# Optimization experiments

Hardware: AMD Instinct MI355X
Metric: run time of the kernel (lower is better)

## Reference

```python
import jax, jax.numpy as jnp
import numpy as np

S, DIM, H = 2048, 1024, 16
D = DIM // H  # head_dim = 64


def rope_rotate_half(x):
    x1, x2 = jnp.split(x, 2, axis=-1)
    return jnp.concatenate([-x2, x1], axis=-1)


def setup_inputs() -> dict:
    key = jax.random.key(0)
    ks = jax.random.split(key, 8)
    x = jax.random.normal(ks[0], (S, DIM), dtype=jnp.float32)
    # RoPE tables for full sequence (HW == S, prefix == 0)
    pos = jnp.arange(S, dtype=jnp.float32)[:, None]
    inv_freq = 1.0 / (10000.0 ** (jnp.arange(0, D, 2, dtype=jnp.float32) / D))
    ang = pos * inv_freq[None, :]                      # [S, D/2]
    ang = jnp.concatenate([ang, ang], axis=-1)         # [S, D]
    sin, cos = jnp.sin(ang), jnp.cos(ang)
    # equinox Linear: weight [out, in], y = W @ x + b
    W_qkv = jax.random.normal(ks[1], (3 * DIM, DIM), dtype=jnp.float32) * (DIM ** -0.5)
    b_qkv = jnp.zeros((3 * DIM,), dtype=jnp.float32)
    W_proj = jax.random.normal(ks[2], (DIM, DIM), dtype=jnp.float32) * (DIM ** -0.5)
    b_proj = jnp.zeros((DIM,), dtype=jnp.float32)
    return {"x": x, "sin": sin, "cos": cos, "W_qkv": W_qkv, "b_qkv": b_qkv,
            "W_proj": W_proj, "b_proj": b_proj}


def reference(x, sin, cos, W_qkv, b_qkv, W_proj, b_proj):
    # fused QKV projection: [S, 3*DIM]
    qkv = x @ W_qkv.T + b_qkv
    # 's (n h d) -> n h s d'
    qkv = qkv.reshape(S, 3, H, D).transpose(1, 2, 0, 3)
    q, k, v = qkv[0], qkv[1], qkv[2]                   # each [H, S, D]
    # qk_norm = False -> Identity. RoPE over all S tokens (prefix = 0).
    sin_b, cos_b = sin[None, :, :], cos[None, :, :]    # [1, S, D]
    q = q * cos_b + rope_rotate_half(q) * sin_b
    k = k * cos_b + rope_rotate_half(k) * sin_b
    attn = jnp.einsum('hqd,hkd->hqk', q, k) / jnp.sqrt(jnp.float32(D))
    attn = jax.nn.softmax(attn, axis=-1)               # [H, S, S]
    out = jnp.einsum('hqk,hkd->hqd', attn, v)          # [H, S, D]
    out = out.transpose(1, 0, 2).reshape(S, DIM)       # 'h s d -> s (h d)'
    return out @ W_proj.T + b_proj
```

## Files before the change

### kernel.cpp

```cpp
#include <hip/hip_runtime.h>

#define S_LEN 2048
#define DIM 1024
#define NH 16
#define HD 64
#define KSPLIT 4

typedef __attribute__((ext_vector_type(8))) __bf16 bf16x8;
typedef __attribute__((ext_vector_type(4))) _Float16 f16x4;
typedef __attribute__((ext_vector_type(4))) float f32x4;
typedef __attribute__((ext_vector_type(8))) unsigned short us8;
typedef __attribute__((ext_vector_type(4))) unsigned short us4;

__device__ __forceinline__ unsigned short f2bf(float f) {
    union { float f; unsigned u; } v; v.f = f;
    unsigned r = v.u + 0x7FFFu + ((v.u >> 16) & 1u);
    return (unsigned short)(r >> 16);
}
__device__ __forceinline__ f32x4 mfma16(bf16x8 a, bf16x8 b, f32x4 c) {
    return __builtin_amdgcn_mfma_f32_16x16x32_bf16(a, b, c, 0, 0, 0);
}
__device__ __forceinline__ f32x4 mfma16h(f16x4 a, f16x4 b, f32x4 c) {
    return __builtin_amdgcn_mfma_f32_16x16x16f16(a, b, c, 0, 0, 0);
}
__device__ __forceinline__ void gload_lds16(void* lds, const void* g) {
    __builtin_amdgcn_global_load_lds(
        (__attribute__((address_space(1))) void*)const_cast<void*>(g),
        (__attribute__((address_space(3))) void*)lds, 16, 0, 0);
}

__global__ __launch_bounds__(256) void convert3_kernel(
    const float* __restrict__ a, unsigned short* __restrict__ oa,
    const float* __restrict__ b, unsigned short* __restrict__ ob,
    const float* __restrict__ c, unsigned short* __restrict__ oc)
{
    const int bid = blockIdx.x;
    const float* in;
    unsigned short* out;
    int i;
    if (bid < 1024)      { in = a; out = oa; i = (bid * 256 + threadIdx.x) * 8; }
    else if (bid < 2560) { in = b; out = ob; i = ((bid - 1024) * 256 + threadIdx.x) * 8; }
    else                 { in = c; out = oc; i = ((bid - 2560) * 256 + threadIdx.x) * 8; }
    const float4 p = *(const float4*)(in + i);
    const float4 q = *(const float4*)(in + i + 4);
    us8 o;
    o[0] = f2bf(p.x); o[1] = f2bf(p.y); o[2] = f2bf(p.z); o[3] = f2bf(p.w);
    o[4] = f2bf(q.x); o[5] = f2bf(q.y); o[6] = f2bf(q.z); o[7] = f2bf(q.w);
    *(us8*)(out + i) = o;
}

__global__ __launch_bounds__(256) void gemm_n128_kernel(
    const unsigned short* __restrict__ A, const unsigned short* __restrict__ B,
    const float* __restrict__ bias, float* __restrict__ C,
    int M, int N, int K)
{
    __shared__ __align__(16) unsigned short As[128 * 32];
    __shared__ __align__(16) unsigned short Bs[128 * 32];

    const int tid  = threadIdx.x;
    const int w    = tid >> 6;
    const int lane = tid & 63;
    const int quad = lane >> 4;
    const int l15  = lane & 15;
    const int bm = blockIdx.y * 128, bn = blockIdx.x * 128;
    const int wm = (w >> 1) * 64,    wn = (w & 1) * 64;
    const int srow = lane >> 2;
    const int skc  = (lane & 3) * 8;

    f32x4 acc[4][4];
    const f32x4 zero4 = {0.f, 0.f, 0.f, 0.f};
    #pragma unroll
    for (int i = 0; i < 4; ++i)
        #pragma unroll
        for (int j = 0; j < 4; ++j) acc[i][j] = zero4;

    for (int k0 = 0; k0 < K; k0 += 32) {
        __syncthreads();
        #pragma unroll
        for (int t = 0; t < 2; ++t) {
            const int row = w * 32 + t * 16 + srow;
            const int ldsoff = (w * 32 + t * 16) * 32;
            gload_lds16(&As[ldsoff], A + (size_t)(bm + row) * K + k0 + skc);
            gload_lds16(&Bs[ldsoff], B + (size_t)(bn + row) * K + k0 + skc);
        }
        __syncthreads();

        bf16x8 a[4], b[4];
        #pragma unroll
        for (int i = 0; i < 4; ++i) {
            a[i] = *(const bf16x8*)&As[(wm + 16 * i + l15) * 32 + quad * 8];
            b[i] = *(const bf16x8*)&Bs[(wn + 16 * i + l15) * 32 + quad * 8];
        }
        #pragma unroll
        for (int i = 0; i < 4; ++i)
            #pragma unroll
            for (int j = 0; j < 4; ++j)
                acc[i][j] = mfma16(a[i], b[j], acc[i][j]);
    }

    #pragma unroll
    for (int j = 0; j < 4; ++j) {
        const int col = bn + wn + 16 * j + l15;
        const float bv = bias[col];
        #pragma unroll
        for (int i = 0; i < 4; ++i)
            #pragma unroll
            for (int r = 0; r < 4; ++r) {
                const int row = bm + wm + 16 * i + quad * 4 + r;
                C[(size_t)row * N + col] = acc[i][j][r] + bv;
            }
    }
}

__global__ __launch_bounds__(256) void gemm_n64_kernel(
    const unsigned short* __restrict__ A, const unsigned short* __restrict__ B,
    const float* __restrict__ bias, float* __restrict__ C,
    int M, int N, int K)
{
    __shared__ __align__(16) unsigned short As[128 * 32];
    __shared__ __align__(16) unsigned short Bs[64 * 32];

    const int tid  = threadIdx.x;
    const int w    = tid >> 6;
    const int lane = tid & 63;
    const int quad = lane >> 4;
    const int l15  = lane & 15;
    const int bm = blockIdx.y * 128, bn = blockIdx.x * 64;
    const int wm = w * 32;
    const int srow = lane >> 2;
    const int skc  = (lane & 3) * 8;

    f32x4 acc[2][4];
    const f32x4 zero4 = {0.f, 0.f, 0.f, 0.f};
    #pragma unroll
    for (int i = 0; i < 2; ++i)
        #pragma unroll
        for (int j = 0; j < 4; ++j) acc[i][j] = zero4;

    for (int k0 = 0; k0 < K; k0 += 32) {
        __syncthreads();
        #pragma unroll
        for (int t = 0; t < 2; ++t) {
            const int row = w * 32 + t * 16 + srow;
            gload_lds16(&As[(w * 32 + t * 16) * 32],
                        A + (size_t)(bm + row) * K + k0 + skc);
        }
        gload_lds16(&Bs[(w * 16) * 32],
                    B + (size_t)(bn + w * 16 + srow) * K + k0 + skc);
        __syncthreads();

        bf16x8 a[2], b[4];
        #pragma unroll
        for (int i = 0; i < 2; ++i)
            a[i] = *(const bf16x8*)&As[(wm + 16 * i + l15) * 32 + quad * 8];
        #pragma unroll
        for (int j = 0; j < 4; ++j)
            b[j] = *(const bf16x8*)&Bs[(16 * j + l15) * 32 + quad * 8];
        #pragma unroll
        for (int i = 0; i < 2; ++i)
            #pragma unroll
            for (int j = 0; j < 4; ++j)
                acc[i][j] = mfma16(a[i], b[j], acc[i][j]);
    }

    #pragma unroll
    for (int j = 0; j < 4; ++j) {
        const int col = bn + 16 * j + l15;
        const float bv = bias[col];
        #pragma unroll
        for (int i = 0; i < 2; ++i)
            #pragma unroll
            for (int r = 0; r < 4; ++r) {
                const int row = bm + wm + 16 * i + quad * 4 + r;
                C[(size_t)row * N + col] = acc[i][j][r] + bv;
            }
    }
}

__global__ __launch_bounds__(256) void rope_vtrans_kernel(
    const float* __restrict__ qkv, const float* __restrict__ sin_t,
    const float* __restrict__ cos_t, unsigned short* __restrict__ Qbf,
    unsigned short* __restrict__ Kbf, _Float16* __restrict__ Vt)
{
    const int bid = blockIdx.x;
    if (bid < 8192) {
        const int idx = bid * 256 + threadIdx.x;
        const int s  = idx >> 10;
        const int r  = idx & 1023;
        const int qk = r >> 9;
        const int h  = (r >> 5) & 15;
        const int d  = r & 31;
        const size_t base = (size_t)s * (3 * DIM) + qk * DIM + h * HD + d;
        const float a = qkv[base];
        const float b = qkv[base + 32];
        const float sv = sin_t[s * HD + d];
        const float cv = cos_t[s * HD + d];
        float ra = a * cv - b * sv;
        float rb = b * cv + a * sv;
        unsigned short* dst = qk ? Kbf : Qbf;
        if (!qk) { ra *= 0.125f; rb *= 0.125f; }
        const size_t o = (size_t)h * S_LEN * HD + (size_t)s * HD + d;
        dst[o]      = f2bf(ra);
        dst[o + 32] = f2bf(rb);
    } else {
        const int vb = bid - 8192;
        const int h  = vb >> 7;
        const int sb = (vb & 127) * 16;
        const int d  = threadIdx.x & 63;
        const int sc = threadIdx.x >> 6;
        const int s0 = sb + sc * 4;
        f16x4 o;
        #pragma unroll
        for (int i = 0; i < 4; ++i)
            o[i] = (_Float16)(qkv[(size_t)(s0 + i) * (3 * DIM) + 2 * DIM + h * HD + d]);
        *(f16x4*)&Vt[(size_t)h * HD * S_LEN + (size_t)d * S_LEN + s0] = o;
    }
}

__global__ __launch_bounds__(256, 4) void attn_mfma_kernel(
    const unsigned short* __restrict__ Qbf, const unsigned short* __restrict__ Kbf,
    const _Float16* __restrict__ Vt, float* __restrict__ Opart,
    float* __restrict__ Lpart)
{
    __shared__ __align__(16) unsigned short Ks[64 * 64];
    __shared__ __align__(16) unsigned short Vts[64 * 64];

    const int h   = blockIdx.y;
    const int qb  = blockIdx.x * 128;
    const int ks  = blockIdx.z;
    const int kb0 = ks * (S_LEN / KSPLIT);
    const int tid  = threadIdx.x;
    const int w    = tid >> 6;
    const int lane = tid & 63;
    const int quad = lane >> 4;
    const int l15  = lane & 15;
    const int t7   = l15 & 7;
    const size_t hoff = (size_t)h * S_LEN * HD;

    bf16x8 aq[2][2];
    #pragma unroll
    for (int g = 0; g < 2; ++g)
        #pragma unroll
        for (int c = 0; c < 2; ++c)
            aq[g][c] = *(const bf16x8*)
                &Qbf[hoff + (size_t)(qb + w * 32 + g * 16 + l15) * HD + 32 * c + quad * 8];

    const f32x4 zero4 = {0.f, 0.f, 0.f, 0.f};
    f32x4 o[2][4];
    #pragma unroll
    for (int g = 0; g < 2; ++g)
        #pragma unroll
        for (int dt = 0; dt < 4; ++dt) o[g][dt] = zero4;
    float lsum[2] = {0.f, 0.f};

    const int r0 = tid >> 3;
    const int c0 = tid & 7;

    for (int kb = 0; kb < S_LEN / KSPLIT; kb += 64) {
        __syncthreads();
        #pragma unroll
        for (int i = 0; i < 2; ++i) {
            const int row = r0 + 32 * i;
            const int sw  = ((c0 ^ (row & 7)) << 3);
            *(us8*)&Ks[row * 64 + sw] =
                *(const us8*)&Kbf[hoff + (size_t)(kb0 + kb + row) * HD + c0 * 8];
            *(us8*)&Vts[row * 64 + sw] =
                *(const us8*)&Vt[hoff + (size_t)row * S_LEN + kb0 + kb + c0 * 8];
        }
        __syncthreads();

        const _Float16* VtsH = (const _Float16*)Vts;
        #pragma unroll
        for (int g = 0; g < 2; ++g) {
            f32x4 s[4];
            #pragma unroll
            for (int kt = 0; kt < 4; ++kt) s[kt] = zero4;
            #pragma unroll
            for (int c = 0; c < 2; ++c)
                #pragma unroll
                for (int kt = 0; kt < 4; ++kt) {
                    const bf16x8 kf = *(const bf16x8*)
                        &Ks[(16 * kt + l15) * 64 + (((4 * c + quad) ^ t7) << 3)];
                    s[kt] = mfma16(kf, aq[g][c], s[kt]);
                }

            f16x4 pb[4];
            #pragma unroll
            for (int kt = 0; kt < 4; ++kt)
                #pragma unroll
                for (int r = 0; r < 4; ++r) {
                    const float p = __expf(s[kt][r]);
                    lsum[g] += p;
                    pb[kt][r] = (_Float16)p;
                }

            #pragma unroll
            for (int kt = 0; kt < 4; ++kt)
                #pragma unroll
                for (int dt = 0; dt < 4; ++dt) {
                    const f16x4 vf = *(const f16x4*)
                        &VtsH[(16 * dt + l15) * 64 +
                              (((2 * kt + (quad >> 1)) ^ t7) << 3) + (quad & 1) * 4];
                    o[g][dt] = mfma16h(pb[kt], vf, o[g][dt]);
                }
        }
    }

    #pragma unroll
    for (int g = 0; g < 2; ++g) {
        lsum[g] += __shfl_xor(lsum[g], 16);
        lsum[g] += __shfl_xor(lsum[g], 32);
        if (lane < 16)
            Lpart[((size_t)ks * NH + h) * S_LEN + qb + w * 32 + g * 16 + l15] = lsum[g];
    }

    #pragma unroll
    for (int g = 0; g < 2; ++g)
        #pragma unroll
        for (int dt = 0; dt < 4; ++dt)
            #pragma unroll
            for (int r = 0; r < 4; ++r) {
                const int row = qb + w * 32 + g * 16 + quad * 4 + r;
                Opart[(size_t)ks * S_LEN * DIM + (size_t)row * DIM +
                      h * HD + 16 * dt + l15] = o[g][dt][r];
            }
}

__global__ __launch_bounds__(256) void combine_kernel(
    const float* __restrict__ Opart, const float* __restrict__ Lpart,
    unsigned short* __restrict__ outb)
{
    const int idx = (blockIdx.x * 256 + threadIdx.x) * 4;
    const int q = idx >> 10, col = idx & 1023, h = col >> 6;
    float l = 0.f;
    float v0 = 0.f, v1 = 0.f, v2 = 0.f, v3 = 0.f;
    #pragma unroll
    for (int ks = 0; ks < KSPLIT; ++ks) {
        l += Lpart[((size_t)ks * NH + h) * S_LEN + q];
        const float4 a = *(const float4*)(Opart + (size_t)ks * S_LEN * DIM + idx);
        v0 += a.x; v1 += a.y; v2 += a.z; v3 += a.w;
    }
    const float rl = 1.0f / l;
    us4 ob;
    ob[0] = f2bf(v0 * rl); ob[1] = f2bf(v1 * rl);
    ob[2] = f2bf(v2 * rl); ob[3] = f2bf(v3 * rl);
    *(us4*)(outb + idx) = ob;
}

extern "C" void kernel_launch(void* const* d_in, const int* in_sizes, int n_in,
                              void* d_out, int out_size, void* d_ws, size_t ws_size,
                              hipStream_t stream) {
    const float* x      = (const float*)d_in[0];
    const float* sin_t  = (const float*)d_in[1];
    const float* cos_t  = (const float*)d_in[2];
    const float* W_qkv  = (const float*)d_in[3];
    const float* b_qkv  = (const float*)d_in[4];
    const float* W_proj = (const float*)d_in[5];
    const float* b_proj = (const float*)d_in[6];
    float* out = (float*)d_out;

    char* ws = (char*)d_ws;
    float* qkv            = (float*)(ws);
    unsigned short* x_bf  = (unsigned short*)(ws + 25165824);
    unsigned short* wq_bf = (unsigned short*)(ws + 29360128);
    float* Opart          = (float*)(ws);
    float* Lpart          = (float*)(ws + 33554432);
    unsigned short* Qbf   = (unsigned short*)(ws + 34078720);
    unsigned short* Kbf   = (unsigned short*)(ws + 38273024);
    _Float16*       Vtbf  = (_Float16*)     (ws + 42467328);
    unsigned short* a_bf  = (unsigned short*)(ws + 34078720);
    unsigned short* wp_bf = (unsigned short*)(ws + 46661632);

    const dim3 blk(256);

    convert3_kernel<<<dim3(3072), blk, 0, stream>>>(
        x, x_bf, W_qkv, wq_bf, W_proj, wp_bf);

    gemm_n128_kernel<<<dim3(24, 16), blk, 0, stream>>>(
        x_bf, wq_bf, b_qkv, qkv, S_LEN, 3 * DIM, DIM);

    rope_vtrans_kernel<<<dim3(10240), blk, 0, stream>>>(
        qkv, sin_t, cos_t, Qbf, Kbf, Vtbf);

    attn_mfma_kernel<<<dim3(16, NH, KSPLIT), blk, 0, stream>>>(
        Qbf, Kbf, Vtbf, Opart, Lpart);

    combine_kernel<<<dim3(2048), blk, 0, stream>>>(Opart, Lpart, a_bf);

    gemm_n64_kernel<<<dim3(16, 16), blk, 0, stream>>>(
        a_bf, wp_bf, b_proj, out, S_LEN, DIM, DIM);
}
```

Before: 174.6 us.

## Store intermediates in bf16, rope in place, prefetch K/V, retile GEMMs

The QKV GEMM now writes bf16 instead of fp32 and uses the 128x64 tile, and RoPE rewrites Q/K in place inside the interleaved qkv buffer, so the separate Q/K buffers go away. Attention reads Q/K straight from that buffer and register-prefetches the next K/V tile, and it writes its partial outputs in bf16. The W_proj conversion moves into the combine kernel, and the projection GEMM uses a smaller 64x64 tile to launch more blocks. Together these cut memory traffic and improve occupancy, at the cost of extra bf16 rounding on qkv and on the partial outputs.

```diff
diff --git a/kernel.cpp b/kernel.cpp
--- a/kernel.cpp
+++ b/kernel.cpp
@@ -17,6 +17,10 @@
     unsigned r = v.u + 0x7FFFu + ((v.u >> 16) & 1u);
     return (unsigned short)(r >> 16);
 }
+__device__ __forceinline__ float bf2f(unsigned short h) {
+    union { unsigned u; float f; } v; v.u = ((unsigned)h) << 16;
+    return v.f;
+}
 __device__ __forceinline__ f32x4 mfma16(bf16x8 a, bf16x8 b, f32x4 c) {
     return __builtin_amdgcn_mfma_f32_16x16x32_bf16(a, b, c, 0, 0, 0);
 }
@@ -29,18 +33,16 @@
         (__attribute__((address_space(3))) void*)lds, 16, 0, 0);
 }
 
-__global__ __launch_bounds__(256) void convert3_kernel(
+__global__ __launch_bounds__(256) void convert2_kernel(
     const float* __restrict__ a, unsigned short* __restrict__ oa,
-    const float* __restrict__ b, unsigned short* __restrict__ ob,
-    const float* __restrict__ c, unsigned short* __restrict__ oc)
+    const float* __restrict__ b, unsigned short* __restrict__ ob)
 {
     const int bid = blockIdx.x;
     const float* in;
     unsigned short* out;
     int i;
-    if (bid < 1024)      { in = a; out = oa; i = (bid * 256 + threadIdx.x) * 8; }
-    else if (bid < 2560) { in = b; out = ob; i = ((bid - 1024) * 256 + threadIdx.x) * 8; }
-    else                 { in = c; out = oc; i = ((bid - 2560) * 256 + threadIdx.x) * 8; }
+    if (bid < 1024) { in = a; out = oa; i = (bid * 256 + threadIdx.x) * 8; }
+    else            { in = b; out = ob; i = ((bid - 1024) * 256 + threadIdx.x) * 8; }
     const float4 p = *(const float4*)(in + i);
     const float4 q = *(const float4*)(in + i + 4);
     us8 o;
@@ -49,72 +51,9 @@
     *(us8*)(out + i) = o;
 }
 
-__global__ __launch_bounds__(256) void gemm_n128_kernel(
+__global__ __launch_bounds__(256) void gemm_qkv_kernel(
     const unsigned short* __restrict__ A, const unsigned short* __restrict__ B,
-    const float* __restrict__ bias, float* __restrict__ C,
-    int M, int N, int K)
-{
-    __shared__ __align__(16) unsigned short As[128 * 32];
-    __shared__ __align__(16) unsigned short Bs[128 * 32];
-
-    const int tid  = threadIdx.x;
-    const int w    = tid >> 6;
-    const int lane = tid & 63;
-    const int quad = lane >> 4;
-    const int l15  = lane & 15;
-    const int bm = blockIdx.y * 128, bn = blockIdx.x * 128;
-    const int wm = (w >> 1) * 64,    wn = (w & 1) * 64;
-    const int srow = lane >> 2;
-    const int skc  = (lane & 3) * 8;
-
-    f32x4 acc[4][4];
-    const f32x4 zero4 = {0.f, 0.f, 0.f, 0.f};
-    #pragma unroll
-    for (int i = 0; i < 4; ++i)
-        #pragma unroll
-        for (int j = 0; j < 4; ++j) acc[i][j] = zero4;
-
-    for (int k0 = 0; k0 < K; k0 += 32) {
-        __syncthreads();
-        #pragma unroll
-        for (int t = 0; t < 2; ++t) {
-            const int row = w * 32 + t * 16 + srow;
-            const int ldsoff = (w * 32 + t * 16) * 32;
-            gload_lds16(&As[ldsoff], A + (size_t)(bm + row) * K + k0 + skc);
-            gload_lds16(&Bs[ldsoff], B + (size_t)(bn + row) * K + k0 + skc);
-        }
-        __syncthreads();
-
-        bf16x8 a[4], b[4];
-        #pragma unroll
-        for (int i = 0; i < 4; ++i) {
-            a[i] = *(const bf16x8*)&As[(wm + 16 * i + l15) * 32 + quad * 8];
-            b[i] = *(const bf16x8*)&Bs[(wn + 16 * i + l15) * 32 + quad * 8];
-        }
-        #pragma unroll
-        for (int i = 0; i < 4; ++i)
-            #pragma unroll
-            for (int j = 0; j < 4; ++j)
-                acc[i][j] = mfma16(a[i], b[j], acc[i][j]);
-    }
-
-    #pragma unroll
-    for (int j = 0; j < 4; ++j) {
-        const int col = bn + wn + 16 * j + l15;
-        const float bv = bias[col];
-        #pragma unroll
-        for (int i = 0; i < 4; ++i)
-            #pragma unroll
-            for (int r = 0; r < 4; ++r) {
-                const int row = bm + wm + 16 * i + quad * 4 + r;
-                C[(size_t)row * N + col] = acc[i][j][r] + bv;
-            }
-    }
-}
-
-__global__ __launch_bounds__(256) void gemm_n64_kernel(
-    const unsigned short* __restrict__ A, const unsigned short* __restrict__ B,
-    const float* __restrict__ bias, float* __restrict__ C,
+    const float* __restrict__ bias, unsigned short* __restrict__ C,
     int M, int N, int K)
 {
     __shared__ __align__(16) unsigned short As[128 * 32];
@@ -172,15 +111,14 @@
             #pragma unroll
             for (int r = 0; r < 4; ++r) {
                 const int row = bm + wm + 16 * i + quad * 4 + r;
-                C[(size_t)row * N + col] = acc[i][j][r] + bv;
+                C[(size_t)row * N + col] = f2bf(acc[i][j][r] + bv);
             }
     }
 }
 
 __global__ __launch_bounds__(256) void rope_vtrans_kernel(
-    const float* __restrict__ qkv, const float* __restrict__ sin_t,
-    const float* __restrict__ cos_t, unsigned short* __restrict__ Qbf,
-    unsigned short* __restrict__ Kbf, _Float16* __restrict__ Vt)
+    unsigned short* __restrict__ qkv, const float* __restrict__ sin_t,
+    const float* __restrict__ cos_t, _Float16* __restrict__ Vt)
 {
     const int bid = blockIdx.x;
     if (bid < 8192) {
@@ -191,17 +129,15 @@
         const int h  = (r >> 5) & 15;
         const int d  = r & 31;
         const size_t base = (size_t)s * (3 * DIM) + qk * DIM + h * HD + d;
-        const float a = qkv[base];
-        const float b = qkv[base + 32];
+        const float a = bf2f(qkv[base]);
+        const float b = bf2f(qkv[base + 32]);
         const float sv = sin_t[s * HD + d];
         const float cv = cos_t[s * HD + d];
         float ra = a * cv - b * sv;
         float rb = b * cv + a * sv;
-        unsigned short* dst = qk ? Kbf : Qbf;
         if (!qk) { ra *= 0.125f; rb *= 0.125f; }
-        const size_t o = (size_t)h * S_LEN * HD + (size_t)s * HD + d;
-        dst[o]      = f2bf(ra);
-        dst[o + 32] = f2bf(rb);
+        qkv[base]      = f2bf(ra);
+        qkv[base + 32] = f2bf(rb);
     } else {
         const int vb = bid - 8192;
         const int h  = vb >> 7;
@@ -212,15 +148,15 @@
         f16x4 o;
         #pragma unroll
         for (int i = 0; i < 4; ++i)
-            o[i] = (_Float16)(qkv[(size_t)(s0 + i) * (3 * DIM) + 2 * DIM + h * HD + d]);
+            o[i] = (_Float16)bf2f(
+                qkv[(size_t)(s0 + i) * (3 * DIM) + 2 * DIM + h * HD + d]);
         *(f16x4*)&Vt[(size_t)h * HD * S_LEN + (size_t)d * S_LEN + s0] = o;
     }
 }
 
 __global__ __launch_bounds__(256, 4) void attn_mfma_kernel(
-    const unsigned short* __restrict__ Qbf, const unsigned short* __restrict__ Kbf,
-    const _Float16* __restrict__ Vt, float* __restrict__ Opart,
-    float* __restrict__ Lpart)
+    const unsigned short* __restrict__ qkv, const unsigned short* __restrict__ VtU,
+    unsigned short* __restrict__ Opart, float* __restrict__ Lpart)
 {
     __shared__ __align__(16) unsigned short Ks[64 * 64];
     __shared__ __align__(16) unsigned short Vts[64 * 64];
@@ -243,7 +179,8 @@
         #pragma unroll
         for (int c = 0; c < 2; ++c)
             aq[g][c] = *(const bf16x8*)
-                &Qbf[hoff + (size_t)(qb + w * 32 + g * 16 + l15) * HD + 32 * c + quad * 8];
+                &qkv[(size_t)(qb + w * 32 + g * 16 + l15) * (3 * DIM) +
+                     h * HD + 32 * c + quad * 8];
 
     const f32x4 zero4 = {0.f, 0.f, 0.f, 0.f};
     f32x4 o[2][4];
@@ -255,6 +192,15 @@
 
     const int r0 = tid >> 3;
     const int c0 = tid & 7;
+
+    us8 pk[2], pv[2];
+    #pragma unroll
+    for (int i = 0; i < 2; ++i) {
+        const int row = r0 + 32 * i;
+        pk[i] = *(const us8*)&qkv[(size_t)(kb0 + row) * (3 * DIM) +
+                                  DIM + h * HD + c0 * 8];
+        pv[i] = *(const us8*)&VtU[hoff + (size_t)row * S_LEN + kb0 + c0 * 8];
+    }
 
     for (int kb = 0; kb < S_LEN / KSPLIT; kb += 64) {
         __syncthreads();
@@ -262,12 +208,21 @@
         for (int i = 0; i < 2; ++i) {
             const int row = r0 + 32 * i;
             const int sw  = ((c0 ^ (row & 7)) << 3);
-            *(us8*)&Ks[row * 64 + sw] =
-                *(const us8*)&Kbf[hoff + (size_t)(kb0 + kb + row) * HD + c0 * 8];
-            *(us8*)&Vts[row * 64 + sw] =
-                *(const us8*)&Vt[hoff + (size_t)row * S_LEN + kb0 + kb + c0 * 8];
-        }
-        __syncthreads();
+            *(us8*)&Ks[row * 64 + sw]  = pk[i];
+            *(us8*)&Vts[row * 64 + sw] = pv[i];
+        }
+        __syncthreads();
+
+        if (kb + 64 < S_LEN / KSPLIT) {
+            #pragma unroll
+            for (int i = 0; i < 2; ++i) {
+                const int row = r0 + 32 * i;
+                pk[i] = *(const us8*)&qkv[(size_t)(kb0 + kb + 64 + row) * (3 * DIM) +
+                                          DIM + h * HD + c0 * 8];
+                pv[i] = *(const us8*)&VtU[hoff + (size_t)row * S_LEN +
+                                          kb0 + kb + 64 + c0 * 8];
+            }
+        }
 
         const _Float16* VtsH = (const _Float16*)Vts;
         #pragma unroll
@@ -322,29 +277,94 @@
             for (int r = 0; r < 4; ++r) {
                 const int row = qb + w * 32 + g * 16 + quad * 4 + r;
                 Opart[(size_t)ks * S_LEN * DIM + (size_t)row * DIM +
-                      h * HD + 16 * dt + l15] = o[g][dt][r];
+                      h * HD + 16 * dt + l15] = f2bf(o[g][dt][r]);
             }
 }
 
 __global__ __launch_bounds__(256) void combine_kernel(
-    const float* __restrict__ Opart, const float* __restrict__ Lpart,
-    unsigned short* __restrict__ outb)
-{
-    const int idx = (blockIdx.x * 256 + threadIdx.x) * 4;
-    const int q = idx >> 10, col = idx & 1023, h = col >> 6;
-    float l = 0.f;
-    float v0 = 0.f, v1 = 0.f, v2 = 0.f, v3 = 0.f;
-    #pragma unroll
-    for (int ks = 0; ks < KSPLIT; ++ks) {
-        l += Lpart[((size_t)ks * NH + h) * S_LEN + q];
-        const float4 a = *(const float4*)(Opart + (size_t)ks * S_LEN * DIM + idx);
-        v0 += a.x; v1 += a.y; v2 += a.z; v3 += a.w;
-    }
-    const float rl = 1.0f / l;
-    us4 ob;
-    ob[0] = f2bf(v0 * rl); ob[1] = f2bf(v1 * rl);
-    ob[2] = f2bf(v2 * rl); ob[3] = f2bf(v3 * rl);
-    *(us4*)(outb + idx) = ob;
+    const unsigned short* __restrict__ Opart, const float* __restrict__ Lpart,
+    unsigned short* __restrict__ outb,
+    const float* __restrict__ Wp, unsigned short* __restrict__ wp_bf)
+{
+    const int bid = blockIdx.x;
+    if (bid < 2048) {
+        const int idx = (bid * 256 + threadIdx.x) * 4;
+        const int q = idx >> 10, col = idx & 1023, h = col >> 6;
+        float l = 0.f;
+        float v0 = 0.f, v1 = 0.f, v2 = 0.f, v3 = 0.f;
+        #pragma unroll
+        for (int ks = 0; ks < KSPLIT; ++ks) {
+            l += Lpart[((size_t)ks * NH + h) * S_LEN + q];
+            const us4 a = *(const us4*)(Opart + (size_t)ks * S_LEN * DIM + idx);
+            v0 += bf2f(a[0]); v1 += bf2f(a[1]); v2 += bf2f(a[2]); v3 += bf2f(a[3]);
+        }
+        const float rl = 1.0f / l;
+        us4 ob;
+        ob[0] = f2bf(v0 * rl); ob[1] = f2bf(v1 * rl);
+        ob[2] = f2bf(v2 * rl); ob[3] = f2bf(v3 * rl);
+        *(us4*)(outb + idx) = ob;
+    } else {
+        const int i = ((bid - 2048) * 256 + threadIdx.x) * 8;
+        const float4 p = *(const float4*)(Wp + i);
+        const float4 q = *(const float4*)(Wp + i + 4);
+        us8 o;
+        o[0] = f2bf(p.x); o[1] = f2bf(p.y); o[2] = f2bf(p.z); o[3] = f2bf(p.w);
+        o[4] = f2bf(q.x); o[5] = f2bf(q.y); o[6] = f2bf(q.z); o[7] = f2bf(q.w);
+        *(us8*)(wp_bf + i) = o;
+    }
+}
+
+__global__ __launch_bounds__(256) void gemm_proj_kernel(
+    const unsigned short* __restrict__ A, const unsigned short* __restrict__ B,
+    const float* __restrict__ bias, float* __restrict__ C,
+    int M, int N, int K)
+{
+    __shared__ __align__(16) unsigned short As[64 * 32];
+    __shared__ __align__(16) unsigned short Bs[64 * 32];
+
+    const int tid  = threadIdx.x;
+    const int w    = tid >> 6;
+    const int lane = tid & 63;
+    const int quad = lane >> 4;
+    const int l15  = lane & 15;
+    const int bm = blockIdx.y * 64, bn = blockIdx.x * 64;
+    const int srow = lane >> 2;
+    const int skc  = (lane & 3) * 8;
+
+    f32x4 acc[4];
+    const f32x4 zero4 = {0.f, 0.f, 0.f, 0.f};
+    #pragma unroll
+    for (int j = 0; j < 4; ++j) acc[j] = zero4;
+
+    for (int k0 = 0; k0 < K; k0 += 32) {
+        __syncthreads();
+        {
+            const int row = w * 16 + srow;
+            gload_lds16(&As[(w * 16) * 32], A + (size_t)(bm + row) * K + k0 + skc);
+            gload_lds16(&Bs[(w * 16) * 32], B + (size_t)(bn + row) * K + k0 + skc);
+        }
+        __syncthreads();
+
+        bf16x8 a, b[4];
+        a = *(const bf16x8*)&As[(w * 16 + l15) * 32 + quad * 8];
+        #pragma unroll
+        for (int j = 0; j < 4; ++j)
+            b[j] = *(const bf16x8*)&Bs[(16 * j + l15) * 32 + quad * 8];
+        #pragma unroll
+        for (int j = 0; j < 4; ++j)
+            acc[j] = mfma16(a, b[j], acc[j]);
+    }
+
+    #pragma unroll
+    for (int j = 0; j < 4; ++j) {
+        const int col = bn + 16 * j + l15;
+        const float bv = bias[col];
+        #pragma unroll
+        for (int r = 0; r < 4; ++r) {
+            const int row = bm + w * 16 + quad * 4 + r;
+            C[(size_t)row * N + col] = acc[j][r] + bv;
+        }
+    }
 }
 
 extern "C" void kernel_launch(void* const* d_in, const int* in_sizes, int n_in,
@@ -360,33 +380,31 @@
     float* out = (float*)d_out;
 
     char* ws = (char*)d_ws;
-    float* qkv            = (float*)(ws);
-    unsigned short* x_bf  = (unsigned short*)(ws + 25165824);
-    unsigned short* wq_bf = (unsigned short*)(ws + 29360128);
-    float* Opart          = (float*)(ws);
-    float* Lpart          = (float*)(ws + 33554432);
-    unsigned short* Qbf   = (unsigned short*)(ws + 34078720);
-    unsigned short* Kbf   = (unsigned short*)(ws + 38273024);
-    _Float16*       Vtbf  = (_Float16*)     (ws + 42467328);
-    unsigned short* a_bf  = (unsigned short*)(ws + 34078720);
-    unsigned short* wp_bf = (unsigned short*)(ws + 46661632);
+    unsigned short* qkv_bf = (unsigned short*)(ws);
+    _Float16*       Vtbf   = (_Float16*)     (ws + 12582912);
+    unsigned short* Opart  = (unsigned short*)(ws + 16777216);
+    float*          Lpart  = (float*)        (ws + 33554432);
+    unsigned short* a_bf   = (unsigned short*)(ws + 34078720);
+    unsigned short* x_bf   = (unsigned short*)(ws + 38273024);
+    unsigned short* wp_bf  = (unsigned short*)(ws + 38273024);
+    unsigned short* wq_bf  = (unsigned short*)(ws + 42467328);
 
     const dim3 blk(256);
 
-    convert3_kernel<<<dim3(3072), blk, 0, stream>>>(
-        x, x_bf, W_qkv, wq_bf, W_proj, wp_bf);
-
-    gemm_n128_kernel<<<dim3(24, 16), blk, 0, stream>>>(
-        x_bf, wq_bf, b_qkv, qkv, S_LEN, 3 * DIM, DIM);
+    convert2_kernel<<<dim3(2560), blk, 0, stream>>>(x, x_bf, W_qkv, wq_bf);
+
+    gemm_qkv_kernel<<<dim3(48, 16), blk, 0, stream>>>(
+        x_bf, wq_bf, b_qkv, qkv_bf, S_LEN, 3 * DIM, DIM);
 
     rope_vtrans_kernel<<<dim3(10240), blk, 0, stream>>>(
-        qkv, sin_t, cos_t, Qbf, Kbf, Vtbf);
+        qkv_bf, sin_t, cos_t, Vtbf);
 
     attn_mfma_kernel<<<dim3(16, NH, KSPLIT), blk, 0, stream>>>(
-        Qbf, Kbf, Vtbf, Opart, Lpart);
-
-    combine_kernel<<<dim3(2048), blk, 0, stream>>>(Opart, Lpart, a_bf);
-
-    gemm_n64_kernel<<<dim3(16, 16), blk, 0, stream>>>(
+        qkv_bf, (const unsigned short*)Vtbf, Opart, Lpart);
+
+    combine_kernel<<<dim3(2560), blk, 0, stream>>>(
+        Opart, Lpart, a_bf, W_proj, wp_bf);
+
+    gemm_proj_kernel<<<dim3(16, 32), blk, 0, stream>>>(
         a_bf, wp_bf, b_proj, out, S_LEN, DIM, DIM);
 }
```

Result: faster. 165.2 us (-5.4%).
